# Kernel tuning notes

Measured on AMD Instinct MI355X. Metric: run time of the kernel, lower is better.

The kernel has to match this reference:

```python
import jax, jax.numpy as jnp
from jax import lax
import numpy as np

P = 7            # patch_size
NP = 10          # n_patches
WIN = 20         # window_size
STRIDE = 4       # window loop stride
EMB = 128        # embedding_dimension
L = WIN - P + 1  # valid-conv output side (14)
HALF = WIN // 2 - P // 2  # window start offset before clipping (7)


def _positions(H, W):
    # x outer, y inner, exactly matching the nested python loops in the source
    return np.array([(x, y) for x in range(0, H - WIN + 1, STRIDE)
                     for y in range(0, W - WIN + 1, STRIDE)], dtype=np.int32)


def _forward(images, Wp, bp, pos_emb, Wb, bb):
    B, C, H, W = images.shape
    BC = B * C
    pos = jnp.asarray(_positions(H, W))  # [Ppos, 2]

    def per_pos(p):
        x, y = p[0], p[1]
        xb0 = jnp.maximum(x - HALF, 0)          # clipped window start (x / cols)
        yb0 = jnp.maximum(y - HALF, 0)          # clipped window start (y / rows)
        winW = jnp.minimum(x - HALF + WIN, W) - xb0  # clipped window width
        winH = jnp.minimum(y - HALF + WIN, H) - yb0  # clipped window height
        # reference patch: rows y:y+P, cols x:x+P (from ORIGINAL data, as in source)
        ref = lax.dynamic_slice(images, (0, 0, y, x), (B, C, P, P)).reshape(BC, 1, P, P)
        # fixed-size window slice; upper bound never clips for our dims, lower-clip
        # handled by masking invalid candidate offsets below
        win = lax.dynamic_slice(images, (0, 0, yb0, xb0), (B, C, WIN, WIN)).reshape(BC, WIN, WIN)
        # grouped cross-correlation == torch conv2d(groups=BC) similarity
        sim = lax.conv_general_dilated(win[None], ref, (1, 1), 'VALID',
                                       feature_group_count=BC,
                                       dimension_numbers=('NCHW', 'OIHW', 'NCHW'))[0]  # [BC,L,L]
        valid = (jnp.arange(L)[:, None] <= winH - P) & (jnp.arange(L)[None, :] <= winW - P)
        sim = jnp.where(valid[None], sim, -jnp.inf)
        _, idx = lax.top_k(sim.reshape(BC, L * L), NP)  # [BC, NP]
        oy, ox = idx // L, idx % L  # row / col offsets inside the window

        def extract(w2, a, b):
            # source's meshgrid indexing yields the TRANSPOSED patch, flattened
            return lax.dynamic_slice(w2, (a, b), (P, P)).T.reshape(P * P)
        patches = jax.vmap(jax.vmap(extract, in_axes=(None, 0, 0)))(win, oy, ox)  # [BC,NP,P*P]
        # source bug kept: x_coords = row offset + x window start (and vice versa)
        return patches, oy + xb0, ox + yb0

    patches, xi, yi = jax.vmap(per_pos)(pos)  # [Ppos,BC,NP,49], [Ppos,BC,NP] int32 x2

    # NOTE: the TransformerEncoder output is discarded in the source; the actual
    # math is back_projection(projection(patches) + pos_emb).
    emb = patches.reshape(-1, B, C, NP, P * P) @ Wp + bp + pos_emb  # [Ppos,B,C,NP,EMB]
    den = (emb @ Wb + bb).reshape(-1, BC, NP, P, P)                 # [Ppos,BC,NP,P,P]

    img0 = images.reshape(BC, H, W)
    cnt0 = jnp.ones((BC, H, W), images.dtype)

    def upd(im, cn, x_i, y_i, d):
        reg = lax.dynamic_slice(im, (y_i, x_i), (P, P))
        c = lax.dynamic_slice(cn, (y_i, x_i), (P, P))
        im = lax.dynamic_update_slice(im, (reg * c + d) / (c + 1.0), (y_i, x_i))
        # source bug kept: counter incremented at transposed slice [x, y]
        ct = lax.dynamic_slice(cn, (x_i, y_i), (P, P)) + 1.0
        cn = lax.dynamic_update_slice(cn, ct, (x_i, y_i))
        return im, cn
    vupd = jax.vmap(upd)  # (b,c) planes are independent -> vectorize

    def n_step(carry, t):
        d, x_i, y_i = t
        return vupd(carry[0], carry[1], x_i, y_i, d), None

    def pos_step(carry, t):
        d, x_i, y_i = t  # d:[BC,NP,P,P]
        carry, _ = lax.scan(n_step, carry, (jnp.moveaxis(d, 1, 0), x_i.T, y_i.T))
        return carry, None

    (img, _), _ = lax.scan(pos_step, (img0, cnt0), (den, xi, yi))
    return img.reshape(B, C, H, W)


def setup_inputs() -> dict:
    key = jax.random.key(0)
    k0, k1, k2, k3 = jax.random.split(key, 4)
    B, C, H, W = 4, 8, 160, 160
    return {
        'images': jax.random.normal(k0, (B, C, H, W), jnp.float32),
        'Wp': jax.random.normal(k1, (P * P, EMB), jnp.float32) * 0.05,
        'bp': jnp.zeros((EMB,), jnp.float32),
        'pos_emb': jax.random.normal(k2, (1, NP, EMB), jnp.float32),
        'Wb': jax.random.normal(k3, (EMB, P * P), jnp.float32) * 0.05,
        'bb': jnp.zeros((P * P,), jnp.float32),
    }


def reference(images, Wp, bp, pos_emb, Wb, bb):
    return _forward(images, Wp, bp, pos_emb, Wb, bb)
```

## Files before the change

kernel.cpp:

```cpp
#include <hip/hip_runtime.h>

#define PS 7
#define NP 10
#define WIN 20
#define STR 4
#define LL 14
#define HALF 7
#define HH 160
#define WW 160
#define BCN 32
#define NX 36
#define PPOS 1296
#define EMBD 128
#define NTASK (BCN * PPOS * NP)
#define NEV (PPOS * NP)
#define CAP 512
#define NTILE 400

__global__ __launch_bounds__(256) void k_mk(const float* __restrict__ Wp,
                                            const float* __restrict__ bp,
                                            const float* __restrict__ pe,
                                            const float* __restrict__ Wb,
                                            const float* __restrict__ bb,
                                            float* __restrict__ M,
                                            float* __restrict__ K) {
    int t = blockIdx.x * 256 + threadIdx.x;
    if (t < 49 * 49) {
        int k = t / 49, d = t % 49;
        float acc = 0.f;
        for (int e = 0; e < EMBD; ++e) acc += Wp[k * EMBD + e] * Wb[e * 49 + d];
        M[t] = acc;
    } else if (t < 49 * 49 + NP * 49) {
        int u = t - 49 * 49;
        int n = u / 49, d = u % 49;
        float acc = bb[d];
        for (int e = 0; e < EMBD; ++e) acc += (bp[e] + pe[n * EMBD + e]) * Wb[e * 49 + d];
        K[u] = acc;
    }
}

__global__ __launch_bounds__(64) void k_sim(const float* __restrict__ img,
                                            unsigned* __restrict__ xy,
                                            float* __restrict__ pd) {
    int blk = blockIdx.x;
    int pos = blk % PPOS;
    int bc  = blk / PPOS;
    int lane = threadIdx.x;
    int ix = pos / NX, iy = pos % NX;
    int x = ix * STR, y = iy * STR;
    int xb0 = max(x - HALF, 0), yb0 = max(y - HALF, 0);
    int jmax = x + 6 - xb0;
    int imax = y + 6 - yb0;
    const float* plane = img + bc * (HH * WW);

    float rf[49];
#pragma unroll
    for (int a = 0; a < PS; ++a)
#pragma unroll
        for (int b = 0; b < PS; ++b)
            rf[a * 7 + b] = plane[(y + a) * WW + (x + b)];

    int B = lane;
    bool bval = B < 56;
    int gr = B / 14, c = B % 14;
    int r0 = gr * 4;
    float acc[4] = {0.f, 0.f, 0.f, 0.f};
    const float* wb = plane + yb0 * WW + xb0 + c;
#pragma unroll
    for (int a = 0; a < 10; ++a) {
        int ra = min(r0 + a, 19);
        const float* rp = wb + ra * WW;
#pragma unroll
        for (int b = 0; b < 7; ++b) {
            float tap = rp[b];
#pragma unroll
            for (int k = 0; k < 4; ++k) {
                int ai = a - k;
                if (ai >= 0 && ai < 7) acc[k] += tap * rf[ai * 7 + b];
            }
        }
    }
    float v[4]; int vidx[4];
#pragma unroll
    for (int k = 0; k < 4; ++k) {
        int rr = r0 + k;
        bool ok = bval && (rr <= imax) && (c <= jmax);
        v[k] = ok ? acc[k] : -INFINITY;
        vidx[k] = rr * 14 + c;
    }

    int a_ = lane / 7, b_ = lane % 7;
    int voffE = b_ * WW + a_;
    bool act = lane < 49;
    int tbase = (bc * PPOS + pos) * NP;

    for (int n = 0; n < NP; ++n) {
        float bv = fmaxf(fmaxf(v[0], v[1]), fmaxf(v[2], v[3]));
#pragma unroll
        for (int off = 32; off >= 1; off >>= 1)
            bv = fmaxf(bv, __shfl_xor(bv, off));
        unsigned long long ms[4];
        ms[0] = __ballot(v[0] == bv);
        ms[1] = __ballot(v[1] == bv);
        ms[2] = __ballot(v[2] == bv);
        ms[3] = __ballot(v[3] == bv);
        int best = 1 << 30, slotw = 0, lanew = 0;
#pragma unroll
        for (int s = 0; s < 4; ++s) {
            if (ms[s]) {
                int l  = __ffsll(ms[s]) - 1;
                int id = __builtin_amdgcn_readlane(vidx[s], l);
                if (id < best) { best = id; slotw = s; lanew = l; }
            }
        }
        int bi = best;
#pragma unroll
        for (int s = 0; s < 4; ++s)
            if (s == slotw && lane == lanew) v[s] = -INFINITY;

        int oy = bi / 14, ox = bi % 14;
        int x_i = oy + xb0;
        int y_i = ox + yb0;
        int t = tbase + n;
        if (lane == 0) xy[t] = (unsigned)x_i | ((unsigned)y_i << 8);
        const float* src = plane + (yb0 + oy) * WW + (xb0 + ox);
        if (act) pd[(size_t)t * 49 + lane] = src[voffE];
    }
}

__global__ __launch_bounds__(256) void k_den(float* __restrict__ pd,
                                             const float* __restrict__ Mg,
                                             const float* __restrict__ Kg) {
    __shared__ float Ps[256 * 49];
    int tid = threadIdx.x;
    size_t base = (size_t)blockIdx.x * (256 * 49);
    for (int i = tid; i < 256 * 49; i += 256) Ps[i] = pd[base + i];
    __syncthreads();

    int t = blockIdx.x * 256 + tid;
    int n = t % NP;
    float acc[49];
#pragma unroll
    for (int d = 0; d < 49; ++d) acc[d] = Kg[n * 49 + d];
    for (int k = 0; k < 49; ++k) {
        float p = Ps[tid * 49 + k];
        const float* mrow = Mg + k * 49;
#pragma unroll
        for (int d = 0; d < 49; ++d) acc[d] += p * mrow[d];
    }
    __syncthreads();
#pragma unroll
    for (int d = 0; d < 49; ++d) Ps[tid * 49 + d] = acc[d];
    __syncthreads();
    for (int i = tid; i < 256 * 49; i += 256) pd[base + i] = Ps[i];
}

__global__ __launch_bounds__(256) void k_apply(const float* __restrict__ img,
                                               const unsigned* __restrict__ xy,
                                               const float* __restrict__ pd,
                                               float* __restrict__ out) {
    __shared__ unsigned lsts[4][CAP];
    int tid  = threadIdx.x;
    int wv   = tid >> 6;
    int lane = tid & 63;
    int gt   = blockIdx.x * 4 + wv;
    int bc   = gt / NTILE;
    int tile = gt % NTILE;
    int tx0 = (tile % 20) * 8, ty0 = (tile / 20) * 8;
    int tx1 = tx0 + 7, ty1 = ty0 + 7;
    const unsigned* xs = xy + bc * NEV;
    unsigned* lst = lsts[wv];

    int a0 = (tx0 <= 19) ? 0 : ((tx0 - 9) >> 2), a1 = min(35, (tx0 + 14) >> 2);
    int b0 = (ty0 <= 19) ? 0 : ((ty0 - 9) >> 2), b1 = min(35, (ty0 + 14) >> 2);
    if (a0 > b0) { int t0 = a0; a0 = b0; b0 = t0; int t1 = a1; a1 = b1; b1 = t1; }
    int lo0 = a0, lo1 = 0, len0, len1;
    if (b0 <= a1 + 1) { len0 = max(a1, b1) - lo0 + 1; len1 = 0; }
    else              { len0 = a1 - a0 + 1; lo1 = b0; len1 = b1 - b0 + 1; }
    int nU = len0 + len1;
    unsigned m = 65536u / (unsigned)nU + 1u;
    int npos = nU * nU;

    unsigned cnt = 0;
    for (int base = 0; base < npos; base += 64) {
        int k = base + lane;
        bool valid = k < npos;
        unsigned kk = valid ? (unsigned)k : 0u;
        int ki = (int)((kk * m) >> 16);
        int kj = (int)kk - ki * nU;
        int ixp = (ki < len0) ? (lo0 + ki) : (lo1 + ki - len0);
        int iyp = (kj < len0) ? (lo0 + kj) : (lo1 + kj - len0);
        int pos = ixp * NX + iyp;
        const unsigned* ep = xs + pos * NP;

        unsigned ev[NP];
#pragma unroll
        for (int n = 0; n < NP; ++n) ev[n] = ep[n];

        unsigned rel = 0;
        unsigned pk[NP];
#pragma unroll
        for (int n = 0; n < NP; ++n) {
            unsigned u = ev[n];
            int x_i = (int)(u & 255u);
            int y_i = (int)((u >> 8) & 255u);
            bool ih = (x_i <= tx1) && (x_i + 6 >= tx0) &&
                      (y_i <= ty1) && (y_i + 6 >= ty0);
            bool ch = (x_i <= ty1) && (x_i + 6 >= ty0) &&
                      (y_i <= tx1) && (y_i + 6 >= tx0);
            bool any = valid && (ih || ch);
            rel |= any ? (1u << n) : 0u;
            pk[n] = (unsigned)(pos * NP + n) | ((unsigned)x_i << 14) | ((unsigned)y_i << 22)
                  | (ih ? (1u << 30) : 0u) | (ch ? (1u << 31) : 0u);
        }
        int myc = __popc(rel);
        int scan = myc;
#pragma unroll
        for (int off = 1; off < 64; off <<= 1) {
            int o = __shfl_up(scan, off);
            scan += (lane >= off) ? o : 0;
        }
        int excl  = (int)cnt + scan - myc;
        int total = __shfl(scan, 63);
        int w = excl;
#pragma unroll
        for (int n = 0; n < NP; ++n) {
            if ((rel >> n) & 1u) { if (w < CAP) lst[w] = pk[n]; ++w; }
        }
        cnt += (unsigned)total;
    }
    if (cnt > CAP) cnt = CAP;
    unsigned cntp = (cnt + 7u) & ~7u;
    if (cntp > CAP) cntp = CAP;
    if (lane < (int)(cntp - cnt)) lst[cnt + lane] = 0u;
    int cntN = (int)cntp;

    int r  = ty0 + (lane >> 3);
    int cc = tx0 + (lane & 7);
    float im = img[bc * (HH * WW) + r * WW + cc];
    float c  = 1.0f;
    const float* ds = pd + (size_t)bc * ((size_t)NEV * 49);
    int vOff = (r * 7 + cc) * 4;

    for (int i = 0; i < cntN; i += 8) {
        unsigned eu[8];
        float    dv[8];
#pragma unroll
        for (int j = 0; j < 8; ++j)
            eu[j] = (unsigned)__builtin_amdgcn_readfirstlane((int)lst[i + j]);
#pragma unroll
        for (int j = 0; j < 8; ++j) {
            unsigned u = eu[j];
            int t    = (int)(u & 16383u);
            int x_i  = (int)((u >> 14) & 255u);
            int y_i  = (int)((u >> 22) & 255u);
            int sOff = (y_i * 7 + x_i) * 4;
            const char* dsb = (const char*)(ds + (size_t)t * 49);
            int boc = min(max(vOff - sOff, 0), 192);
            dv[j] = *(const float*)(dsb + boc);
        }
#pragma unroll
        for (int j = 0; j < 8; ++j) {
            unsigned u = eu[j];
            int x_i = (int)((u >> 14) & 255u);
            int y_i = (int)((u >> 22) & 255u);
            int dr = r - y_i, dc = cc - x_i;
            bool h = (u & (1u << 30)) && (((unsigned)dr <= 6u) & ((unsigned)dc <= 6u));
            float nim = fmaf(im, c, dv[j]) * __builtin_amdgcn_rcpf(c + 1.0f);
            im = h ? nim : im;
            int er = r - x_i, ec = cc - y_i;
            bool hc = (u >> 31) && (((unsigned)er <= 6u) & ((unsigned)ec <= 6u));
            c += hc ? 1.0f : 0.0f;
        }
    }
    out[bc * (HH * WW) + r * WW + cc] = im;
}

extern "C" void kernel_launch(void* const* d_in, const int* in_sizes, int n_in,
                              void* d_out, int out_size, void* d_ws, size_t ws_size,
                              hipStream_t stream) {
    const float* img = (const float*)d_in[0];
    const float* Wp  = (const float*)d_in[1];
    const float* bp  = (const float*)d_in[2];
    const float* pe  = (const float*)d_in[3];
    const float* Wb  = (const float*)d_in[4];
    const float* bb  = (const float*)d_in[5];
    float* out = (float*)d_out;

    float* wsf = (float*)d_ws;
    float*    M   = wsf;
    float*    K   = wsf + 2404;
    unsigned* xy  = (unsigned*)(wsf + 2896);
    float*    pd  = wsf + 2896 + NTASK;

    k_mk<<<12, 256, 0, stream>>>(Wp, bp, pe, Wb, bb, M, K);
    k_sim<<<BCN * PPOS, 64, 0, stream>>>(img, xy, pd);
    k_den<<<NTASK / 256, 256, 0, stream>>>(pd, M, K);
    k_apply<<<BCN * NTILE / 4, 256, 0, stream>>>(img, xy, pd, out);
}
```

Measured before the change: 315.6 us.

## Fuse patch denoising matmul into similarity kernel, drop separate k_den pass

The 49x49 patch transform (M matrix plus per-slot bias K) now runs inside k_sim right after each top-k patch is selected, and the k_den kernel is removed. Each lane keeps one column of M in registers and computes one output element with 49 FMAs, reading the transposed patch directly from the image. This removes a full write-then-read round trip of the patch buffer through global memory and one kernel launch. In exchange k_sim carries 49 more registers per lane and does its per-lane patch reads uncoalesced inside the top-k loop.

```diff
diff --git a/kernel.cpp b/kernel.cpp
--- a/kernel.cpp
+++ b/kernel.cpp
@@ -40,6 +40,8 @@
 }
 
 __global__ __launch_bounds__(64) void k_sim(const float* __restrict__ img,
+                                            const float* __restrict__ Mg,
+                                            const float* __restrict__ Kg,
                                             unsigned* __restrict__ xy,
                                             float* __restrict__ pd) {
     int blk = blockIdx.x;
@@ -89,8 +91,11 @@
         vidx[k] = rr * 14 + c;
     }
 
-    int a_ = lane / 7, b_ = lane % 7;
-    int voffE = b_ * WW + a_;
+    int ld = min(lane, 48);
+    float Mc[49];
+#pragma unroll
+    for (int j = 0; j < 49; ++j) Mc[j] = Mg[j * 49 + ld];
+
     bool act = lane < 49;
     int tbase = (bc * PPOS + pos) * NP;
 
@@ -124,35 +129,12 @@
         int t = tbase + n;
         if (lane == 0) xy[t] = (unsigned)x_i | ((unsigned)y_i << 8);
         const float* src = plane + (yb0 + oy) * WW + (xb0 + ox);
-        if (act) pd[(size_t)t * 49 + lane] = src[voffE];
-    }
-}
-
-__global__ __launch_bounds__(256) void k_den(float* __restrict__ pd,
-                                             const float* __restrict__ Mg,
-                                             const float* __restrict__ Kg) {
-    __shared__ float Ps[256 * 49];
-    int tid = threadIdx.x;
-    size_t base = (size_t)blockIdx.x * (256 * 49);
-    for (int i = tid; i < 256 * 49; i += 256) Ps[i] = pd[base + i];
-    __syncthreads();
-
-    int t = blockIdx.x * 256 + tid;
-    int n = t % NP;
-    float acc[49];
-#pragma unroll
-    for (int d = 0; d < 49; ++d) acc[d] = Kg[n * 49 + d];
-    for (int k = 0; k < 49; ++k) {
-        float p = Ps[tid * 49 + k];
-        const float* mrow = Mg + k * 49;
-#pragma unroll
-        for (int d = 0; d < 49; ++d) acc[d] += p * mrow[d];
-    }
-    __syncthreads();
-#pragma unroll
-    for (int d = 0; d < 49; ++d) Ps[tid * 49 + d] = acc[d];
-    __syncthreads();
-    for (int i = tid; i < 256 * 49; i += 256) pd[base + i] = Ps[i];
+        float den = Kg[n * 49 + ld];
+#pragma unroll
+        for (int j = 0; j < 49; ++j)
+            den = fmaf(src[(j % 7) * WW + (j / 7)], Mc[j], den);
+        if (act) pd[(size_t)t * 49 + lane] = den;
+    }
 }
 
 __global__ __launch_bounds__(256) void k_apply(const float* __restrict__ img,
@@ -294,7 +276,6 @@
     float*    pd  = wsf + 2896 + NTASK;
 
     k_mk<<<12, 256, 0, stream>>>(Wp, bp, pe, Wb, bb, M, K);
-    k_sim<<<BCN * PPOS, 64, 0, stream>>>(img, xy, pd);
-    k_den<<<NTASK / 256, 256, 0, stream>>>(pd, M, K);
+    k_sim<<<BCN * PPOS, 64, 0, stream>>>(img, M, K, xy, pd);
     k_apply<<<BCN * NTILE / 4, 256, 0, stream>>>(img, xy, pd, out);
 }
```

Result: faster. 300.1 us (-4.9%).
